# Kernel optimization log

Hardware: AMD Instinct MI355X
Metric: run time of the kernel (lower is better)

Reference implementation:

```python
import jax, jax.numpy as jnp
import numpy as np

K = 0.1            # manifold curvature param: points satisfy <x,x>_L = -1/K
H = 8              # num_heads
DH = 64            # head_spatial_dim
SP = 512           # spatial_dim = H*DH
SCALE = 1.0 / np.sqrt(DH)
SQRT_K = np.sqrt(K).astype(np.float32)


def _lorentz_fc(x, W, b):
    # Manifold-constrained FC: linear map to spatial coords, time recomputed
    sp = x @ W + b                                            # [..., out_spatial]
    t = jnp.sqrt(jnp.clip(1.0 / K + jnp.sum(sp * sp, axis=-1, keepdims=True), 1e-9, None))
    return jnp.concatenate([t, sp], axis=-1)


def _logmap0(p):
    # Lorentz log map at origin -> tangent spatial coords (time comp = 0)
    t, sp = p[..., :1], p[..., 1:]
    nrm = jnp.sqrt(jnp.sum(sp * sp, axis=-1, keepdims=True))
    theta = jnp.arccosh(jnp.clip(SQRT_K * t, 1.0 + 1e-7, None))
    return (theta / SQRT_K) * sp / jnp.maximum(nrm, 1e-9)


def _expmap0(u):
    nrm = jnp.sqrt(jnp.sum(u * u, axis=-1, keepdims=True))
    t = jnp.cosh(SQRT_K * nrm) / SQRT_K
    sp = jnp.sinh(SQRT_K * nrm) * u / (SQRT_K * jnp.maximum(nrm, 1e-9))
    return jnp.concatenate([t, sp], axis=-1)


def setup_inputs() -> dict:
    key = jax.random.key(0)
    ks = jax.random.split(key, 9)
    B, N = 4, 2048
    space = jax.random.normal(ks[0], (B, N, SP), dtype=jnp.float32) * 0.5
    t = jnp.sqrt(1.0 / K + jnp.sum(space * space, axis=-1, keepdims=True))
    x = jnp.concatenate([t, space], axis=-1)                  # on-manifold [B,N,513]
    s = (1 + SP) ** -0.5
    Wq = jax.random.normal(ks[1], (1 + SP, SP), dtype=jnp.float32) * s
    Wk = jax.random.normal(ks[2], (1 + SP, SP), dtype=jnp.float32) * s
    Wv = jax.random.normal(ks[3], (1 + SP, SP), dtype=jnp.float32) * s
    Wo = jax.random.normal(ks[4], (1 + SP, SP), dtype=jnp.float32) * s
    bq = jax.random.normal(ks[5], (SP,), dtype=jnp.float32) * 0.01
    bk = jax.random.normal(ks[6], (SP,), dtype=jnp.float32) * 0.01
    bv = jax.random.normal(ks[7], (SP,), dtype=jnp.float32) * 0.01
    bo = jax.random.normal(ks[8], (SP,), dtype=jnp.float32) * 0.01
    return {"x": x, "Wq": Wq, "bq": bq, "Wk": Wk, "bk": bk, "Wv": Wv, "bv": bv, "Wo": Wo, "bo": bo}


def _split_heads(p):
    # [B,N,1+H*DH] -> [B,H,N,1+DH], sharing the time component across heads
    B, N, _ = p.shape
    t = p[..., :1]                                            # [B,N,1]
    sp = p[..., 1:].reshape(B, N, H, DH)
    t = jnp.broadcast_to(t[:, :, None, :], (B, N, H, 1))
    return jnp.concatenate([t, sp], axis=-1).transpose(0, 2, 1, 3)


def reference(x, Wq, bq, Wk, bk, Wv, bv, Wo, bo):
    q = _split_heads(_lorentz_fc(x, Wq, bq))                  # [B,H,N,1+DH]
    k = _split_heads(_lorentz_fc(x, Wk, bk))
    v = _split_heads(_lorentz_fc(x, Wv, bv))
    # Lorentzian inner product scores: -q_t k_t + <q_s, k_s>
    scores = (jnp.einsum('bhnd,bhmd->bhnm', q[..., 1:], k[..., 1:])
              - jnp.einsum('bhni,bhmi->bhnm', q[..., :1], k[..., :1])) * SCALE
    attn = jax.nn.softmax(scores, axis=-1)                    # [B,H,N,N]
    # Riemannian aggregation: logmap0 -> weighted sum in tangent space -> expmap0
    v_tan = _logmap0(v)                                       # [B,H,N,DH]
    out_tan = jnp.einsum('bhnm,bhmd->bhnd', attn, v_tan)
    out = _expmap0(out_tan)                                   # [B,H,N,1+DH]
    # direct head concat: stack spatial parts, renormalize time onto manifold
    B, _, N, _ = out.shape
    space_cat = out[..., 1:].transpose(0, 2, 1, 3).reshape(B, N, H * DH)
    t_prime = jnp.sqrt(jnp.clip(1.0 / K + jnp.sum(space_cat * space_cat, axis=-1, keepdims=True), 1e-9, None))
    cat = jnp.concatenate([t_prime, space_cat], axis=-1)      # [B,N,513]
    return _lorentz_fc(cat, Wo, bo)                           # [B,N,513]
```

## Files before the change

### kernel.cpp

```cpp
#include <hip/hip_runtime.h>
#include <math.h>

#define H_    8
#define DH_   64
#define SPD   512
#define NSEQ  2048
#define BATCH 4
#define ROWS  8192
#define KDIM  513
#define INVK  10.0f
#define SQRTK 0.31622776601683794f
#define S2C   0.18033688011112043f
#define LOG2E 1.4426950408889634f
#define TKOFF 12.0f

using bf16x8 = __attribute__((ext_vector_type(8))) short;
using f32x4  = __attribute__((ext_vector_type(4))) float;
using f32x16 = __attribute__((ext_vector_type(16))) float;

static __device__ __forceinline__ short f2bf(float f){
  union { float f; unsigned u; } v; v.f = f;
  unsigned r = v.u + 0x7fffu + ((v.u >> 16) & 1u);
  return (short)(r >> 16);
}
static __device__ __forceinline__ float bf2f(short s){
  union { unsigned u; float f; } v; v.u = ((unsigned)(unsigned short)s) << 16;
  return v.f;
}
static __device__ __forceinline__ unsigned cvtpk(float lo, float hi){
  unsigned r; asm("v_cvt_pk_bf16_f32 %0, %1, %2" : "=v"(r) : "v"(lo), "v"(hi)); return r;
}
static __device__ __forceinline__ void plswapu(unsigned& a, unsigned& b){
  asm("v_permlane32_swap_b32 %0, %1" : "+v"(a), "+v"(b));
}
static __device__ __forceinline__ float exp2v(float x){
  float r; asm("v_exp_f32 %0, %1" : "=v"(r) : "v"(x)); return r;
}

#define GL16(gp, lp) __builtin_amdgcn_global_load_lds( \
    (const __attribute__((address_space(1))) void*)(gp), \
    (__attribute__((address_space(3))) void*)(lp), 16, 0, 0)

__global__ __launch_bounds__(256) void convx_kernel(const float* __restrict__ x,
                                                    short* __restrict__ xs){
  const int i2 = (blockIdx.x * 256 + threadIdx.x) * 2;
  const int r = i2 >> 9, c = i2 & 511;
  const float a = x[(size_t)r * KDIM + 1 + c];
  const float b = x[(size_t)r * KDIM + 2 + c];
  const unsigned pk = (unsigned)(unsigned short)f2bf(a) |
                      ((unsigned)(unsigned short)f2bf(b) << 16);
  *(unsigned*)(xs + (size_t)r * SPD + c) = pk;
}

__global__ __launch_bounds__(256) void convw_kernel(const float* __restrict__ Wq,
                                                    const float* __restrict__ Wk,
                                                    const float* __restrict__ Wv,
                                                    const float* __restrict__ Wo,
                                                    short* __restrict__ WT){
  const int wsel = blockIdx.y;
  const float* W = (wsel == 0) ? Wq : (wsel == 1) ? Wk : (wsel == 2) ? Wv : Wo;
  const int i = blockIdx.x * 256 + threadIdx.x;
  const int n = i >> 9, k = i & 511;
  WT[(size_t)wsel * SPD * SPD + i] = f2bf(W[(size_t)(k + 1) * SPD + n]);
}

template<bool BF16OUT, int BM>
__global__ __launch_bounds__(256) void gemm_kernel(
    const short* __restrict__ A, const short* __restrict__ WTbase,
    int sel0, int sel1, int sel2,
    const float* __restrict__ bias0, const float* __restrict__ bias1,
    const float* __restrict__ bias2,
    const float* __restrict__ W00, const float* __restrict__ W01,
    const float* __restrict__ W02,
    const float* __restrict__ tvec, long tstride,
    void* __restrict__ C0, void* __restrict__ C1, void* __restrict__ C2,
    int ldc, int coff)
{
  constexpr int NREP = (BM == 128) ? 4 : 2;
  const int z = blockIdx.z;
  const int sel = (z == 0) ? sel0 : (z == 1) ? sel1 : sel2;
  const short* BT = WTbase + (size_t)sel * SPD * SPD;
  const float* bias = (z == 0) ? bias0 : (z == 1) ? bias1 : bias2;
  const float* W0 = (z == 0) ? W00 : (z == 1) ? W01 : W02;
  void* C = (z == 0) ? C0 : (z == 1) ? C1 : C2;

  __shared__ short As[BM * 32];
  __shared__ short Bs[128 * 32];

  const int tid  = threadIdx.x;
  const int lane = tid & 63;
  const int wave = tid >> 6;
  const int row0 = blockIdx.x * BM;
  const int col0 = blockIdx.y * 128;
  const int wr = (BM == 128) ? (wave >> 1) * 64 : 0;
  const int wc = (BM == 128) ? (wave & 1) * 64 : wave * 32;
  const int rA  = lane & 15;
  const int kg2 = (lane >> 4) * 16;
  const int g4  = lane >> 4;

  f32x4 acc[4][NREP] = {};

  for (int kt = 0; kt < SPD / 32; ++kt){
    __syncthreads();
    #pragma unroll
    for (int p = 0; p < BM / 64; ++p){
      const int idx = p * 256 + tid;
      const int r = idx >> 2, c4 = idx & 3;
      const int gc = (c4 ^ ((r >> 1) & 3)) * 8;
      GL16(A + (size_t)(row0 + r) * SPD + kt * 32 + gc, (char*)As + idx * 16);
    }
    #pragma unroll
    for (int p = 0; p < 2; ++p){
      const int idx = p * 256 + tid;
      const int r = idx >> 2, c4 = idx & 3;
      const int gc = (c4 ^ ((r >> 1) & 3)) * 8;
      GL16(BT + (size_t)(col0 + r) * SPD + kt * 32 + gc, (char*)Bs + idx * 16);
    }
    asm volatile("s_waitcnt vmcnt(0)" ::: "memory");
    __syncthreads();
    bf16x8 af[4], bfr[NREP];
    #pragma unroll
    for (int m = 0; m < 4; ++m){
      const int r = wr + m * 16 + rA;
      af[m] = *(const bf16x8*)((const char*)As + ((r * 64 + kg2) ^ (((r >> 1) & 3) << 4)));
    }
    #pragma unroll
    for (int n = 0; n < NREP; ++n){
      const int r = wc + n * 16 + rA;
      bfr[n] = *(const bf16x8*)((const char*)Bs + ((r * 64 + kg2) ^ (((r >> 1) & 3) << 4)));
    }
    #pragma unroll
    for (int m = 0; m < 4; ++m)
      #pragma unroll
      for (int n = 0; n < NREP; ++n)
        acc[m][n] = __builtin_amdgcn_mfma_f32_16x16x32_bf16(af[m], bfr[n], acc[m][n], 0, 0, 0);
  }

  float trow[4][4];
  #pragma unroll
  for (int m = 0; m < 4; ++m)
    #pragma unroll
    for (int j = 0; j < 4; ++j)
      trow[m][j] = tvec[(size_t)(row0 + wr + m * 16 + g4 * 4 + j) * tstride];

  #pragma unroll
  for (int m = 0; m < 4; ++m){
    const int row = row0 + wr + m * 16 + g4 * 4;
    #pragma unroll
    for (int n = 0; n < NREP; ++n){
      const int col = col0 + wc + n * 16 + rA;
      const float bv = bias[col];
      const float w0 = W0[col];
      #pragma unroll
      for (int j = 0; j < 4; ++j){
        const float v = acc[m][n][j] + trow[m][j] * w0 + bv;
        if (BF16OUT) ((short*)C)[(size_t)(row + j) * SPD + col] = f2bf(v);
        else         ((float*)C)[(size_t)(row + j) * ldc + coff + col] = v;
      }
    }
  }
}

__global__ __launch_bounds__(256) void postqkv_kernel(
    const short* __restrict__ qb, const short* __restrict__ kb,
    const short* __restrict__ vb, float* __restrict__ tq,
    unsigned* __restrict__ tkpk, short* __restrict__ vtT)
{
  const int tid = threadIdx.x;
  const int lane = tid & 63;
  const int wv = tid >> 6;
  const int row0 = blockIdx.x * 8 + wv * 2;
  const int b = blockIdx.x >> 8;

  #pragma unroll
  for (int i = 0; i < 2; ++i){
    const int row = row0 + i;
    const int n = row & (NSEQ - 1);
    {
      union { bf16x8 v; short e[8]; } u;
      u.v = *(const bf16x8*)(qb + (size_t)row * SPD + lane * 8);
      float s = 0.f;
      #pragma unroll
      for (int j = 0; j < 8; ++j){ const float f = bf2f(u.e[j]); s += f * f; }
      #pragma unroll
      for (int m = 1; m <= 32; m <<= 1) s += __shfl_xor(s, m, 64);
      if (lane == 0) tq[row] = sqrtf(INVK + s);
    }
    {
      union { bf16x8 v; short e[8]; } u;
      u.v = *(const bf16x8*)(kb + (size_t)row * SPD + lane * 8);
      float s = 0.f;
      #pragma unroll
      for (int j = 0; j < 8; ++j){ const float f = bf2f(u.e[j]); s += f * f; }
      #pragma unroll
      for (int m = 1; m <= 32; m <<= 1) s += __shfl_xor(s, m, 64);
      if (lane == 0){
        const float tkm = sqrtf(INVK + s) - TKOFF;
        const short bhi = f2bf(tkm);
        const short blo = f2bf(tkm - bf2f(bhi));
        tkpk[row] = (unsigned)(unsigned short)bhi | ((unsigned)(unsigned short)blo << 16);
      }
    }
    {
      union { bf16x8 v; short e[8]; } u;
      u.v = *(const bf16x8*)(vb + (size_t)row * SPD + lane * 8);
      float f[8]; float sh = 0.f;
      #pragma unroll
      for (int j = 0; j < 8; ++j){ f[j] = bf2f(u.e[j]); sh += f[j] * f[j]; }
      sh += __shfl_xor(sh, 1, 64);
      sh += __shfl_xor(sh, 2, 64);
      sh += __shfl_xor(sh, 4, 64);
      float tot = sh;
      tot += __shfl_xor(tot, 8, 64);
      tot += __shfl_xor(tot, 16, 64);
      tot += __shfl_xor(tot, 32, 64);
      const float tv = sqrtf(INVK + tot);
      const float av = fmaxf(SQRTK * tv, 1.0f + 1e-7f);
      const float theta = __logf(av + sqrtf(av * av - 1.0f));
      const float fac = theta * (1.0f / SQRTK);
      const float inv = fac / fmaxf(sqrtf(sh), 1e-9f);
      const int h = lane >> 3;
      const int d0 = (lane & 7) * 8;
      short* dst = vtT + ((size_t)((b * H_ + h) * DH_ + d0)) * NSEQ + n;
      #pragma unroll
      for (int j = 0; j < 8; ++j) dst[(size_t)j * NSEQ] = f2bf(inv * f[j]);
    }
  }
}

__global__ __launch_bounds__(256) void attn_kernel(
    const short* __restrict__ qb, const short* __restrict__ kb,
    const short* __restrict__ vtT, const float* __restrict__ tqg,
    const unsigned* __restrict__ tkpk, short* __restrict__ catb)
{
  int bid = blockIdx.x;
  bid = (bid & 7) * 64 + (bid >> 3);
  const int qt = bid & 15;
  const int bh = bid >> 4;
  const int b = bh >> 3, h = bh & 7;
  const int q0 = qt * 128;
  const int tid = threadIdx.x;
  const int lane = tid & 63;
  const int w = tid >> 6;
  const int l31 = lane & 31;
  const int hi = lane >> 5;
  const int rsw = (l31 & 7) << 4;

  __shared__ short Ks[2][64 * 64];
  __shared__ short Vs[2][64 * 64];
  __shared__ float lred[4][32];
  __shared__ unsigned tks[NSEQ];

  const int qrow = q0 + w * 32 + l31;
  bf16x8 qf[4];
  {
    const short* qptr = qb + (size_t)(b * NSEQ + qrow) * SPD + h * DH_ + hi * 8;
    #pragma unroll
    for (int s = 0; s < 4; ++s){
      union { bf16x8 v; short e[8]; } u;
      u.v = *(const bf16x8*)(qptr + s * 16);
      #pragma unroll
      for (int j = 0; j < 8; ++j) u.e[j] = f2bf(bf2f(u.e[j]) * S2C);
      qf[s] = u.v;
    }
  }
  bf16x8 qf4;
  {
    const float a = -S2C * tqg[b * NSEQ + qrow];
    const short ahi = f2bf(a);
    const short alo = f2bf(a - bf2f(ahi));
    union { unsigned u[4]; bf16x8 v; } q4;
    q4.u[0] = hi ? 0u : ((unsigned)(unsigned short)ahi | ((unsigned)(unsigned short)alo << 16));
    q4.u[1] = hi ? 0u : (unsigned)(unsigned short)ahi;
    q4.u[2] = 0; q4.u[3] = 0;
    qf4 = q4.v;
  }
  bf16x8 onesB;
  {
    const unsigned val = (l31 == 0) ? 0x3f803f80u : 0u;
    union { unsigned u[4]; bf16x8 v; } ob;
    ob.u[0] = val; ob.u[1] = val; ob.u[2] = val; ob.u[3] = val;
    onesB = ob.v;
  }

  {
    const unsigned* tsrc = tkpk + b * NSEQ + tid * 8;
    *(uint4*)&tks[tid * 8]     = *(const uint4*)tsrc;
    *(uint4*)&tks[tid * 8 + 4] = *(const uint4*)(tsrc + 4);
  }

  const int rB = tid >> 3;
  const int c0 = (tid & 7) * 16;
  const int cc = c0 ^ ((rB & 7) << 4);
  const short* kbase = kb + (size_t)(b * NSEQ) * SPD + h * DH_;
  const short* vbase = vtT + (size_t)(bh * DH_) * NSEQ;

  uint4 kA0, kA1, vA0, vA1;
  uint4 kB0, kB1, vB0, vB1;

#define LOADA(m0) do{ \
    kA0 = *(const uint4*)(kbase + (size_t)((m0) + rB) * SPD + (c0 >> 1)); \
    kA1 = *(const uint4*)(kbase + (size_t)((m0) + 32 + rB) * SPD + (c0 >> 1)); \
    vA0 = *(const uint4*)(vbase + (size_t)rB * NSEQ + (m0) + (c0 >> 1)); \
    vA1 = *(const uint4*)(vbase + (size_t)(32 + rB) * NSEQ + (m0) + (c0 >> 1)); }while(0)
#define LOADB(m0) do{ \
    kB0 = *(const uint4*)(kbase + (size_t)((m0) + rB) * SPD + (c0 >> 1)); \
    kB1 = *(const uint4*)(kbase + (size_t)((m0) + 32 + rB) * SPD + (c0 >> 1)); \
    vB0 = *(const uint4*)(vbase + (size_t)rB * NSEQ + (m0) + (c0 >> 1)); \
    vB1 = *(const uint4*)(vbase + (size_t)(32 + rB) * NSEQ + (m0) + (c0 >> 1)); }while(0)
#define WRITEA(buf) do{ \
    *(uint4*)((char*)Ks[buf] + rB * 128 + cc) = kA0; \
    *(uint4*)((char*)Ks[buf] + (32 + rB) * 128 + cc) = kA1; \
    *(uint4*)((char*)Vs[buf] + rB * 128 + cc) = vA0; \
    *(uint4*)((char*)Vs[buf] + (32 + rB) * 128 + cc) = vA1; }while(0)
#define WRITEB(buf) do{ \
    *(uint4*)((char*)Ks[buf] + rB * 128 + cc) = kB0; \
    *(uint4*)((char*)Ks[buf] + (32 + rB) * 128 + cc) = kB1; \
    *(uint4*)((char*)Vs[buf] + rB * 128 + cc) = vB0; \
    *(uint4*)((char*)Vs[buf] + (32 + rB) * 128 + cc) = vB1; }while(0)
#define BARRIER() asm volatile("s_waitcnt lgkmcnt(0)\n\ts_barrier" ::: "memory")
#define WAITV4()  asm volatile("s_waitcnt vmcnt(4)" ::: "memory")
#define WAITV0()  asm volatile("s_waitcnt vmcnt(0)" ::: "memory")

  f32x16 o[2] = {};
  f32x16 lacc = {};

  auto KAUG = [&](unsigned pk)->bf16x8{
    union { unsigned u[4]; bf16x8 v; } ka;
    ka.u[0] = hi ? 0u : ((pk & 0xFFFFu) | (pk << 16));
    ka.u[1] = hi ? 0u : (pk >> 16);
    ka.u[2] = 0; ka.u[3] = 0;
    return ka.v;
  };

  auto COMPUTE = [&](const char* Kc, const char* Vc, int m0){
    const unsigned pk0 = tks[m0 + l31];
    const unsigned pk1 = tks[m0 + 32 + l31];

    f32x16 sacc[2] = {};
    __builtin_amdgcn_s_setprio(1);
    #pragma unroll
    for (int f = 0; f < 2; ++f){
      const int rowb = (f * 32 + l31) * 128;
      #pragma unroll
      for (int s = 0; s < 4; ++s){
        const bf16x8 kf = *(const bf16x8*)(Kc + rowb + ((s * 32 + hi * 16) ^ rsw));
        sacc[f] = __builtin_amdgcn_mfma_f32_32x32x16_bf16(kf, qf[s], sacc[f], 0, 0, 0);
      }
    }
    sacc[0] = __builtin_amdgcn_mfma_f32_32x32x16_bf16(KAUG(pk0), qf4, sacc[0], 0, 0, 0);
    sacc[1] = __builtin_amdgcn_mfma_f32_32x32x16_bf16(KAUG(pk1), qf4, sacc[1], 0, 0, 0);
    __builtin_amdgcn_s_setprio(0);

    #pragma unroll
    for (int f = 0; f < 2; ++f)
      #pragma unroll
      for (int e = 0; e < 16; ++e)
        sacc[f][e] = exp2v(sacc[f][e]);

    bf16x8 pa[4];
    #pragma unroll
    for (int f = 0; f < 2; ++f)
      #pragma unroll
      for (int g16 = 0; g16 < 2; ++g16){
        const int bse = g16 * 8;
        unsigned A0 = cvtpk(sacc[f][bse + 0], sacc[f][bse + 1]);
        unsigned A1 = cvtpk(sacc[f][bse + 2], sacc[f][bse + 3]);
        unsigned B0 = cvtpk(sacc[f][bse + 4], sacc[f][bse + 5]);
        unsigned B1 = cvtpk(sacc[f][bse + 6], sacc[f][bse + 7]);
        plswapu(A0, B0);
        plswapu(A1, B1);
        union { unsigned u[4]; bf16x8 v; } pu;
        pu.u[0] = A0; pu.u[1] = A1; pu.u[2] = B0; pu.u[3] = B1;
        pa[f * 2 + g16] = pu.v;
      }

    __builtin_amdgcn_s_setprio(1);
    #pragma unroll
    for (int db = 0; db < 2; ++db){
      const int rowb = (db * 32 + l31) * 128;
      #pragma unroll
      for (int ks = 0; ks < 4; ++ks){
        const bf16x8 vf = *(const bf16x8*)(Vc + rowb + ((ks * 32 + hi * 16) ^ rsw));
        o[db] = __builtin_amdgcn_mfma_f32_32x32x16_bf16(pa[ks], vf, o[db], 0, 0, 0);
      }
    }
    #pragma unroll
    for (int ks = 0; ks < 4; ++ks)
      lacc = __builtin_amdgcn_mfma_f32_32x32x16_bf16(pa[ks], onesB, lacc, 0, 0, 0);
    __builtin_amdgcn_s_setprio(0);
  };

  LOADA(0);
  WAITV0();
  WRITEA(0);
  __syncthreads();
  LOADB(64);

  const int NT = NSEQ / 64;
  #pragma unroll 1
  for (int t = 0; t < NT; t += 2){
    const int m0 = t * 64;
    if (t + 2 < NT) LOADA(m0 + 128);
    COMPUTE((const char*)Ks[0], (const char*)Vs[0], m0);
    if (t + 2 < NT) WAITV4(); else WAITV0();
    WRITEB(1);
    BARRIER();
    if (t + 3 < NT) LOADB(m0 + 192);
    COMPUTE((const char*)Ks[1], (const char*)Vs[1], m0 + 64);
    if (t + 2 < NT){
      if (t + 3 < NT) WAITV4(); else WAITV0();
      WRITEA(0);
    }
    BARRIER();
  }

  if (l31 == 0){
    #pragma unroll
    for (int e = 0; e < 16; ++e)
      lred[w][(e & 3) + 8 * (e >> 2) + 4 * hi] = lacc[e];
  }
  asm volatile("s_waitcnt lgkmcnt(0)" ::: "memory");
  f32x4 lv[4];
  #pragma unroll
  for (int g = 0; g < 4; ++g) lv[g] = *(const f32x4*)&lred[w][8 * g + 4 * hi];

  const size_t obase = (size_t)(b * NSEQ + q0 + w * 32) * SPD + h * DH_ + l31;
  #pragma unroll
  for (int e = 0; e < 16; ++e){
    const float linv = __builtin_amdgcn_rcpf(lv[e >> 2][e & 3]);
    const float ov0 = o[0][e] * linv;
    const float ov1 = o[1][e] * linv;
    float ss = ov0 * ov0 + ov1 * ov1;
    #pragma unroll
    for (int off = 16; off; off >>= 1) ss += __shfl_xor(ss, off, 64);
    const float nrm = sqrtf(ss);
    const float e2 = exp2f(SQRTK * nrm * LOG2E);
    const float einv = __builtin_amdgcn_rcpf(e2);
    const float fac = (e2 - einv) * 0.5f * __builtin_amdgcn_rcpf(SQRTK * fmaxf(nrm, 1e-9f));
    const int crow = (e & 3) + 8 * (e >> 2) + 4 * hi;
    catb[obase + (size_t)crow * SPD]      = f2bf(fac * ov0);
    catb[obase + (size_t)crow * SPD + 32] = f2bf(fac * ov1);
  }
#undef LOADA
#undef LOADB
#undef WRITEA
#undef WRITEB
#undef BARRIER
#undef WAITV4
#undef WAITV0
}

__global__ __launch_bounds__(256) void tp_kernel(const short* __restrict__ catb,
                                                 float* __restrict__ tps){
  const int lane = threadIdx.x & 63;
  const int row = blockIdx.x * 4 + (threadIdx.x >> 6);
  union { bf16x8 v; short e[8]; } u;
  u.v = *(const bf16x8*)(catb + (size_t)row * SPD + lane * 8);
  float s = 0.f;
  #pragma unroll
  for (int j = 0; j < 8; ++j){ const float f = bf2f(u.e[j]); s += f * f; }
  #pragma unroll
  for (int m = 1; m <= 32; m <<= 1) s += __shfl_xor(s, m, 64);
  if (lane == 0) tps[row] = sqrtf(fmaxf(INVK + s, 1e-9f));
}

__global__ __launch_bounds__(256) void fin_kernel(float* __restrict__ out){
  const int lane = threadIdx.x & 63;
  const int row = blockIdx.x * 4 + (threadIdx.x >> 6);
  const float* rp = out + (size_t)row * KDIM + 1;
  float s = 0.f;
  #pragma unroll
  for (int j = 0; j < 8; ++j){ const float f = rp[j * 64 + lane]; s += f * f; }
  #pragma unroll
  for (int m = 1; m <= 32; m <<= 1) s += __shfl_xor(s, m, 64);
  if (lane == 0) out[(size_t)row * KDIM] = sqrtf(fmaxf(INVK + s, 1e-9f));
}

extern "C" void kernel_launch(void* const* d_in, const int* in_sizes, int n_in,
                              void* d_out, int out_size, void* d_ws, size_t ws_size,
                              hipStream_t stream)
{
  (void)in_sizes; (void)n_in; (void)out_size; (void)ws_size;
  const float* x  = (const float*)d_in[0];
  const float* Wq = (const float*)d_in[1];
  const float* bq = (const float*)d_in[2];
  const float* Wk = (const float*)d_in[3];
  const float* bk = (const float*)d_in[4];
  const float* Wv = (const float*)d_in[5];
  const float* bv = (const float*)d_in[6];
  const float* Wo = (const float*)d_in[7];
  const float* bo = (const float*)d_in[8];
  float* out = (float*)d_out;

  char* p = (char*)d_ws;
  short* xs   = (short*)p; p += (size_t)ROWS * SPD * 2;
  short* WT   = (short*)p; p += (size_t)4 * SPD * SPD * 2;
  short* qb   = (short*)p; p += (size_t)ROWS * SPD * 2;
  short* kb   = (short*)p; p += (size_t)ROWS * SPD * 2;
  short* vb   = (short*)p; p += (size_t)ROWS * SPD * 2;
  short* vtT  = (short*)p; p += (size_t)ROWS * SPD * 2;
  float* tq   = (float*)p; p += (size_t)ROWS * 4;
  unsigned* tkpk = (unsigned*)p; p += (size_t)ROWS * 4;
  short* catb = (short*)p; p += (size_t)ROWS * SPD * 2;
  float* tps  = (float*)p; p += (size_t)ROWS * 4;

  convx_kernel<<<(ROWS * SPD / 2) / 256, 256, 0, stream>>>(x, xs);
  convw_kernel<<<dim3((SPD * SPD) / 256, 4), 256, 0, stream>>>(Wq, Wk, Wv, Wo, WT);
  gemm_kernel<true, 128><<<dim3(64, 4, 3), 256, 0, stream>>>(
      xs, WT, 0, 1, 2, bq, bk, bv, Wq, Wk, Wv, x, (long)KDIM,
      qb, kb, vb, SPD, 0);
  postqkv_kernel<<<1024, 256, 0, stream>>>(qb, kb, vb, tq, tkpk, vtT);
  attn_kernel<<<512, 256, 0, stream>>>(qb, kb, vtT, tq, tkpk, catb);
  tp_kernel<<<ROWS / 4, 256, 0, stream>>>(catb, tps);
  gemm_kernel<false, 64><<<dim3(128, 4, 1), 256, 0, stream>>>(
      catb, WT, 3, 3, 3, bo, bo, bo, Wo, Wo, Wo, tps, 1L,
      out, out, out, KDIM, 1);
  fin_kernel<<<ROWS / 4, 256, 0, stream>>>(out);
}
```

Baseline: 146.4 us.

## Fuse row sum-of-squares into attention and output GEMM epilogues, merge conversion kernels

```diff
diff --git a/kernel.cpp b/kernel.cpp
--- a/kernel.cpp
+++ b/kernel.cpp
@@ -41,30 +41,33 @@
     (const __attribute__((address_space(1))) void*)(gp), \
     (__attribute__((address_space(3))) void*)(lp), 16, 0, 0)
 
-__global__ __launch_bounds__(256) void convx_kernel(const float* __restrict__ x,
-                                                    short* __restrict__ xs){
-  const int i2 = (blockIdx.x * 256 + threadIdx.x) * 2;
-  const int r = i2 >> 9, c = i2 & 511;
-  const float a = x[(size_t)r * KDIM + 1 + c];
-  const float b = x[(size_t)r * KDIM + 2 + c];
-  const unsigned pk = (unsigned)(unsigned short)f2bf(a) |
-                      ((unsigned)(unsigned short)f2bf(b) << 16);
-  *(unsigned*)(xs + (size_t)r * SPD + c) = pk;
-}
-
-__global__ __launch_bounds__(256) void convw_kernel(const float* __restrict__ Wq,
-                                                    const float* __restrict__ Wk,
-                                                    const float* __restrict__ Wv,
-                                                    const float* __restrict__ Wo,
-                                                    short* __restrict__ WT){
-  const int wsel = blockIdx.y;
-  const float* W = (wsel == 0) ? Wq : (wsel == 1) ? Wk : (wsel == 2) ? Wv : Wo;
-  const int i = blockIdx.x * 256 + threadIdx.x;
-  const int n = i >> 9, k = i & 511;
-  WT[(size_t)wsel * SPD * SPD + i] = f2bf(W[(size_t)(k + 1) * SPD + n]);
-}
-
-template<bool BF16OUT, int BM>
+__global__ __launch_bounds__(256) void conv_kernel(const float* __restrict__ x,
+                                                   const float* __restrict__ Wq,
+                                                   const float* __restrict__ Wk,
+                                                   const float* __restrict__ Wv,
+                                                   const float* __restrict__ Wo,
+                                                   short* __restrict__ xs,
+                                                   short* __restrict__ WT){
+  const int bid = blockIdx.x;
+  if (bid < 8192){
+    const int i2 = (bid * 256 + threadIdx.x) * 2;
+    const int r = i2 >> 9, c = i2 & 511;
+    const float a = x[(size_t)r * KDIM + 1 + c];
+    const float b = x[(size_t)r * KDIM + 2 + c];
+    const unsigned pk = (unsigned)(unsigned short)f2bf(a) |
+                        ((unsigned)(unsigned short)f2bf(b) << 16);
+    *(unsigned*)(xs + (size_t)r * SPD + c) = pk;
+  } else {
+    const int q = bid - 8192;
+    const int wsel = q >> 10;
+    const float* W = (wsel == 0) ? Wq : (wsel == 1) ? Wk : (wsel == 2) ? Wv : Wo;
+    const int i = (q & 1023) * 256 + threadIdx.x;
+    const int n = i >> 9, k = i & 511;
+    WT[(size_t)wsel * SPD * SPD + i] = f2bf(W[(size_t)(k + 1) * SPD + n]);
+  }
+}
+
+template<bool BF16OUT, int BM, bool TSQ, bool FUSESSQ>
 __global__ __launch_bounds__(256) void gemm_kernel(
     const short* __restrict__ A, const short* __restrict__ WTbase,
     int sel0, int sel1, int sel2,
@@ -73,6 +76,7 @@
     const float* __restrict__ W00, const float* __restrict__ W01,
     const float* __restrict__ W02,
     const float* __restrict__ tvec, long tstride,
+    float* __restrict__ ssqout,
     void* __restrict__ C0, void* __restrict__ C1, void* __restrict__ C2,
     int ldc, int coff)
 {
@@ -140,8 +144,16 @@
   #pragma unroll
   for (int m = 0; m < 4; ++m)
     #pragma unroll
-    for (int j = 0; j < 4; ++j)
-      trow[m][j] = tvec[(size_t)(row0 + wr + m * 16 + g4 * 4 + j) * tstride];
+    for (int j = 0; j < 4; ++j){
+      const float raw = tvec[(size_t)(row0 + wr + m * 16 + g4 * 4 + j) * tstride];
+      trow[m][j] = TSQ ? sqrtf(fmaxf(INVK + raw, 1e-9f)) : raw;
+    }
+
+  float rssq[4][4];
+  #pragma unroll
+  for (int m = 0; m < 4; ++m)
+    #pragma unroll
+    for (int j = 0; j < 4; ++j) rssq[m][j] = 0.f;
 
   #pragma unroll
   for (int m = 0; m < 4; ++m){
@@ -154,10 +166,24 @@
       #pragma unroll
       for (int j = 0; j < 4; ++j){
         const float v = acc[m][n][j] + trow[m][j] * w0 + bv;
+        if (FUSESSQ) rssq[m][j] += v * v;
         if (BF16OUT) ((short*)C)[(size_t)(row + j) * SPD + col] = f2bf(v);
         else         ((float*)C)[(size_t)(row + j) * ldc + coff + col] = v;
       }
     }
+  }
+  if (FUSESSQ){
+    #pragma unroll
+    for (int m = 0; m < 4; ++m)
+      #pragma unroll
+      for (int j = 0; j < 4; ++j){
+        float s = rssq[m][j];
+        s += __shfl_xor(s, 1, 64);
+        s += __shfl_xor(s, 2, 64);
+        s += __shfl_xor(s, 4, 64);
+        s += __shfl_xor(s, 8, 64);
+        if (rA == 0) atomicAdd(&ssqout[row0 + wr + m * 16 + g4 * 4 + j], s);
+      }
   }
 }
 
@@ -231,7 +257,8 @@
 __global__ __launch_bounds__(256) void attn_kernel(
     const short* __restrict__ qb, const short* __restrict__ kb,
     const short* __restrict__ vtT, const float* __restrict__ tqg,
-    const unsigned* __restrict__ tkpk, short* __restrict__ catb)
+    const unsigned* __restrict__ tkpk, short* __restrict__ catb,
+    float* __restrict__ tps)
 {
   int bid = blockIdx.x;
   bid = (bid & 7) * 64 + (bid >> 3);
@@ -288,6 +315,13 @@
     *(uint4*)&tks[tid * 8]     = *(const uint4*)tsrc;
     *(uint4*)&tks[tid * 8 + 4] = *(const uint4*)(tsrc + 4);
   }
+
+  int koff[2][4];
+  #pragma unroll
+  for (int f = 0; f < 2; ++f)
+    #pragma unroll
+    for (int s = 0; s < 4; ++s)
+      koff[f][s] = (f * 32 + l31) * 128 + ((s * 32 + hi * 16) ^ rsw);
 
   const int rB = tid >> 3;
   const int c0 = (tid & 7) * 16;
@@ -324,6 +358,7 @@
 
   f32x16 o[2] = {};
   f32x16 lacc = {};
+  const f32x16 z16 = {};
 
   auto KAUG = [&](unsigned pk)->bf16x8{
     union { unsigned u[4]; bf16x8 v; } ka;
@@ -337,14 +372,17 @@
     const unsigned pk0 = tks[m0 + l31];
     const unsigned pk1 = tks[m0 + 32 + l31];
 
-    f32x16 sacc[2] = {};
+    f32x16 sacc[2];
     __builtin_amdgcn_s_setprio(1);
     #pragma unroll
     for (int f = 0; f < 2; ++f){
-      const int rowb = (f * 32 + l31) * 128;
-      #pragma unroll
-      for (int s = 0; s < 4; ++s){
-        const bf16x8 kf = *(const bf16x8*)(Kc + rowb + ((s * 32 + hi * 16) ^ rsw));
+      {
+        const bf16x8 kf = *(const bf16x8*)(Kc + koff[f][0]);
+        sacc[f] = __builtin_amdgcn_mfma_f32_32x32x16_bf16(kf, qf[0], z16, 0, 0, 0);
+      }
+      #pragma unroll
+      for (int s = 1; s < 4; ++s){
+        const bf16x8 kf = *(const bf16x8*)(Kc + koff[f][s]);
         sacc[f] = __builtin_amdgcn_mfma_f32_32x32x16_bf16(kf, qf[s], sacc[f], 0, 0, 0);
       }
     }
@@ -377,14 +415,12 @@
 
     __builtin_amdgcn_s_setprio(1);
     #pragma unroll
-    for (int db = 0; db < 2; ++db){
-      const int rowb = (db * 32 + l31) * 128;
+    for (int db = 0; db < 2; ++db)
       #pragma unroll
       for (int ks = 0; ks < 4; ++ks){
-        const bf16x8 vf = *(const bf16x8*)(Vc + rowb + ((ks * 32 + hi * 16) ^ rsw));
+        const bf16x8 vf = *(const bf16x8*)(Vc + koff[db][ks]);
         o[db] = __builtin_amdgcn_mfma_f32_32x32x16_bf16(pa[ks], vf, o[db], 0, 0, 0);
       }
-    }
     #pragma unroll
     for (int ks = 0; ks < 4; ++ks)
       lacc = __builtin_amdgcn_mfma_f32_32x32x16_bf16(pa[ks], onesB, lacc, 0, 0, 0);
@@ -425,7 +461,8 @@
   #pragma unroll
   for (int g = 0; g < 4; ++g) lv[g] = *(const f32x4*)&lred[w][8 * g + 4 * hi];
 
-  const size_t obase = (size_t)(b * NSEQ + q0 + w * 32) * SPD + h * DH_ + l31;
+  const int brow = b * NSEQ + q0 + w * 32;
+  const size_t obase = (size_t)brow * SPD + h * DH_ + l31;
   #pragma unroll
   for (int e = 0; e < 16; ++e){
     const float linv = __builtin_amdgcn_rcpf(lv[e >> 2][e & 3]);
@@ -441,6 +478,7 @@
     const int crow = (e & 3) + 8 * (e >> 2) + 4 * hi;
     catb[obase + (size_t)crow * SPD]      = f2bf(fac * ov0);
     catb[obase + (size_t)crow * SPD + 32] = f2bf(fac * ov1);
+    if (l31 == 0) atomicAdd(&tps[brow + crow], fac * fac * ss);
   }
 #undef LOADA
 #undef LOADB
@@ -451,30 +489,10 @@
 #undef WAITV0
 }
 
-__global__ __launch_bounds__(256) void tp_kernel(const short* __restrict__ catb,
-                                                 float* __restrict__ tps){
-  const int lane = threadIdx.x & 63;
-  const int row = blockIdx.x * 4 + (threadIdx.x >> 6);
-  union { bf16x8 v; short e[8]; } u;
-  u.v = *(const bf16x8*)(catb + (size_t)row * SPD + lane * 8);
-  float s = 0.f;
-  #pragma unroll
-  for (int j = 0; j < 8; ++j){ const float f = bf2f(u.e[j]); s += f * f; }
-  #pragma unroll
-  for (int m = 1; m <= 32; m <<= 1) s += __shfl_xor(s, m, 64);
-  if (lane == 0) tps[row] = sqrtf(fmaxf(INVK + s, 1e-9f));
-}
-
-__global__ __launch_bounds__(256) void fin_kernel(float* __restrict__ out){
-  const int lane = threadIdx.x & 63;
-  const int row = blockIdx.x * 4 + (threadIdx.x >> 6);
-  const float* rp = out + (size_t)row * KDIM + 1;
-  float s = 0.f;
-  #pragma unroll
-  for (int j = 0; j < 8; ++j){ const float f = rp[j * 64 + lane]; s += f * f; }
-  #pragma unroll
-  for (int m = 1; m <= 32; m <<= 1) s += __shfl_xor(s, m, 64);
-  if (lane == 0) out[(size_t)row * KDIM] = sqrtf(fmaxf(INVK + s, 1e-9f));
+__global__ __launch_bounds__(256) void fin2_kernel(float* __restrict__ out,
+                                                   const float* __restrict__ tos){
+  const int r = blockIdx.x * 256 + threadIdx.x;
+  out[(size_t)r * KDIM] = sqrtf(fmaxf(INVK + tos[r], 1e-9f));
 }
 
 extern "C" void kernel_launch(void* const* d_in, const int* in_sizes, int n_in,
@@ -504,17 +522,17 @@
   unsigned* tkpk = (unsigned*)p; p += (size_t)ROWS * 4;
   short* catb = (short*)p; p += (size_t)ROWS * SPD * 2;
   float* tps  = (float*)p; p += (size_t)ROWS * 4;
-
-  convx_kernel<<<(ROWS * SPD / 2) / 256, 256, 0, stream>>>(x, xs);
-  convw_kernel<<<dim3((SPD * SPD) / 256, 4), 256, 0, stream>>>(Wq, Wk, Wv, Wo, WT);
-  gemm_kernel<true, 128><<<dim3(64, 4, 3), 256, 0, stream>>>(
-      xs, WT, 0, 1, 2, bq, bk, bv, Wq, Wk, Wv, x, (long)KDIM,
+  float* tos  = (float*)p; p += (size_t)ROWS * 4;
+
+  hipMemsetAsync(tps, 0, (size_t)2 * ROWS * 4, stream);
+  conv_kernel<<<8192 + 4096, 256, 0, stream>>>(x, Wq, Wk, Wv, Wo, xs, WT);
+  gemm_kernel<true, 128, false, false><<<dim3(64, 4, 3), 256, 0, stream>>>(
+      xs, WT, 0, 1, 2, bq, bk, bv, Wq, Wk, Wv, x, (long)KDIM, nullptr,
       qb, kb, vb, SPD, 0);
   postqkv_kernel<<<1024, 256, 0, stream>>>(qb, kb, vb, tq, tkpk, vtT);
-  attn_kernel<<<512, 256, 0, stream>>>(qb, kb, vtT, tq, tkpk, catb);
-  tp_kernel<<<ROWS / 4, 256, 0, stream>>>(catb, tps);
-  gemm_kernel<false, 64><<<dim3(128, 4, 1), 256, 0, stream>>>(
-      catb, WT, 3, 3, 3, bo, bo, bo, Wo, Wo, Wo, tps, 1L,
+  attn_kernel<<<512, 256, 0, stream>>>(qb, kb, vtT, tq, tkpk, catb, tps);
+  gemm_kernel<false, 64, true, true><<<dim3(128, 4, 1), 256, 0, stream>>>(
+      catb, WT, 3, 3, 3, bo, bo, bo, Wo, Wo, Wo, tps, 1L, tos,
       out, out, out, KDIM, 1);
-  fin_kernel<<<ROWS / 4, 256, 0, stream>>>(out);
-}
+  fin2_kernel<<<ROWS / 256, 256, 0, stream>>>(out, tos);
+}
```

Result: no change. 149.0 us (+1.8%).
